# Kernel optimization log

Hardware: AMD Instinct MI355X
Metric: run time of the kernel (lower is better)

Reference implementation:

```python
import jax, jax.numpy as jnp
import numpy as np

D_MODEL = 1024
STATE_DIM = 16
BATCH = 32
SEQ = 2048


def setup_inputs() -> dict:
    key = jax.random.key(0)
    k_x, k_win, k_bin, k_wout, k_bout = jax.random.split(key, 5)
    proj_dim = 2 * D_MODEL + 3 * STATE_DIM
    x = jax.random.normal(k_x, (BATCH, SEQ, D_MODEL), dtype=jnp.float32)
    # Dense kernels (glorot-ish scale) and zero biases, as in fresh keras layers
    W_in = jax.random.normal(k_win, (D_MODEL, proj_dim), dtype=jnp.float32) * 0.02
    b_in = jnp.zeros((proj_dim,), dtype=jnp.float32)
    W_out = jax.random.normal(k_wout, (D_MODEL, D_MODEL), dtype=jnp.float32) * 0.02
    b_out = jnp.zeros((D_MODEL,), dtype=jnp.float32)
    # A_log init: -log([1..state_dim])
    A_log = -jnp.log(jnp.arange(1, STATE_DIM + 1, dtype=jnp.float32))
    return {"x": x, "W_in": W_in, "b_in": b_in, "A_log": A_log,
            "W_out": W_out, "b_out": b_out}


def _selective_scan(delta, A, B, C):
    # delta, B, C: [b, s, n]; A: [n]
    # state_t = exp(A * delta_t) * state_{t-1} + B_t ; y_t = sum(state_t * C_t)
    def step(state, inp):
        delta_t, B_t, C_t = inp  # each [b, n]
        state = jnp.exp(A * delta_t) * state + B_t
        y = jnp.sum(state * C_t, axis=-1)  # [b]
        return state, y

    b = delta.shape[0]
    init = jnp.zeros((b, A.shape[0]), dtype=delta.dtype)
    # scan over time: move seq axis to front -> [s, b, n]
    xs = (jnp.swapaxes(delta, 0, 1), jnp.swapaxes(B, 0, 1), jnp.swapaxes(C, 0, 1))
    _, ys = jax.lax.scan(step, init, xs)  # ys: [s, b]
    return jnp.swapaxes(ys, 0, 1)  # [b, s]


def reference(x, W_in, b_in, A_log, W_out, b_out):
    xz = jnp.einsum('bsd,dp->bsp', x, W_in) + b_in  # [b, s, 2*d + 3*n]
    d, n = D_MODEL, STATE_DIM
    xm = xz[..., :d]                     # unused by scan (matches original)
    z = xz[..., d:2 * d]                 # [b, s, d]
    Bm = xz[..., 2 * d:2 * d + n]        # [b, s, n]
    Cm = xz[..., 2 * d + n:2 * d + 2 * n]
    delta = jax.nn.softplus(xz[..., 2 * d + 2 * n:])  # [b, s, n]
    A = -jnp.exp(A_log)                  # [n]
    y = _selective_scan(delta, A, Bm, Cm)  # [b, s]
    y = y[..., None] * jax.nn.gelu(z, approximate=False)  # [b, s, d]
    return jnp.einsum('bsd,de->bse', y, W_out) + b_out
```

## Files before the change

### kernel.cpp

```cpp
#include <hip/hip_runtime.h>
#include <cstdint>

typedef float fx4 __attribute__((ext_vector_type(4)));
typedef short sx8 __attribute__((ext_vector_type(8)));
typedef short sx4 __attribute__((ext_vector_type(4)));

#define NSTATE 16
#define SEQ_LEN 2048
#define NBATCH 32
#define MROWS 65536
#define KDIM 1024
#define N1 1072
#define N1PAD 1152
#define BK 32
#define NSTEP (KDIM / BK)
#define TILE_SHORTS 4096
#define TSTRIDE (NSTEP * TILE_SHORTS)
#define RING 4
#define SLOT_SHORTS 8192

__device__ __forceinline__ short f2bf(float f) {
  unsigned u = __float_as_uint(f);
  u += 0x7FFFu + ((u >> 16) & 1u);
  return (short)(u >> 16);
}

__device__ __forceinline__ float gelu_exact(float x) {
  float ax = fabsf(x) * 0.70710678118654752f;
  float t = __builtin_amdgcn_rcpf(fmaf(0.3275911f, ax, 1.0f));
  float p = fmaf(1.061405429f, t, -1.453152027f);
  p = fmaf(p, t, 1.421413741f);
  p = fmaf(p, t, -0.284496736f);
  p = fmaf(p, t, 0.254829592f);
  p = p * t;
  float e = __expf(-ax * ax);
  float erfv = fmaf(-p, e, 1.0f);
  erfv = copysignf(erfv, x);
  return 0.5f * x * (1.0f + erfv);
}

#define GLOAD_LDS16(gp, lp)                                                          \
  __builtin_amdgcn_global_load_lds(                                                  \
      (const __attribute__((address_space(1))) unsigned int*)(gp),                   \
      (__attribute__((address_space(3))) unsigned int*)(lp), 16, 0, 0)

#define SBAR() do { __builtin_amdgcn_s_barrier(); asm volatile("" ::: "memory"); } while (0)
#define WAITLGKM0() asm volatile("s_waitcnt lgkmcnt(0)" ::: "memory")

__global__ void convert_pack_x(const float* __restrict__ x, short* __restrict__ xbp) {
  const int wave = threadIdx.x >> 6;
  const int lane = threadIdx.x & 63;
  const int r0 = blockIdx.x * 64 + wave * 16;
  const int q = (lane & 7) >> 1;
  const int eo = (lane & 1) * 4;
  const int kt0 = lane >> 3;
  for (int r16 = 0; r16 < 16; ++r16) {
    const int m = r0 + r16;
    const int rloc = m & 127;
    const long pbase = ((long)(m >> 7) * NSTEP) * TILE_SHORTS + rloc * 32;
    const int p8 = (((q + (rloc >> 1)) & 3)) * 8 + eo;
#pragma unroll
    for (int seg = 0; seg < 4; ++seg) {
      fx4 v = *(const fx4*)(x + (long)m * KDIM + seg * 256 + lane * 4);
      sx4 o;
      o[0] = f2bf(v[0]); o[1] = f2bf(v[1]); o[2] = f2bf(v[2]); o[3] = f2bf(v[3]);
      *(sx4*)(xbp + pbase + (long)(seg * 8 + kt0) * TILE_SHORTS + p8) = o;
    }
  }
}

__global__ void transpose_w_kernel(const float* __restrict__ src, short* __restrict__ dst,
                                   int src_cols, int col_off, int valid_rows) {
  __shared__ float t[32][33];
  int j0 = blockIdx.x * 32;
  int k0 = blockIdx.y * 32;
  int c = threadIdx.x & 31;
  int r = threadIdx.x >> 5;
#pragma unroll
  for (int i = 0; i < 4; i++) {
    int k = k0 + r + i * 8;
    int j = j0 + c;
    float v = (j < valid_rows) ? src[(long)k * src_cols + col_off + j] : 0.f;
    t[r + i * 8][c] = v;
  }
  __syncthreads();
#pragma unroll
  for (int i = 0; i < 4; i++) {
    int n = j0 + r + i * 8;
    int k = k0 + c;
    int rr = n & 127;
    long addr = ((long)(n >> 7) * NSTEP + (k >> 5)) * TILE_SHORTS + rr * 32
              + ((((k >> 3) & 3) + ((rr >> 1) & 3)) & 3) * 8 + (k & 7);
    dst[addr] = f2bf(t[c][r + i * 8]);
  }
}

__device__ __forceinline__ void gemm_mainloop256(const short* __restrict__ Abase,
                                                 const short* __restrict__ Bbase,
                                                 short* lds, fx4 acc[4][4]) {
  const int tid = threadIdx.x;
  const int lane = tid & 63;
  const int wave = tid >> 6;
  const int wm = wave >> 2, wn = wave & 3;
  const int l15 = lane & 15, ks = lane >> 4;

#pragma unroll
  for (int i = 0; i < 4; i++)
#pragma unroll
    for (int j = 0; j < 4; j++) acc[i][j] = fx4{0.f, 0.f, 0.f, 0.f};

  short* AshR = lds;
  short* BshR = lds + RING * SLOT_SHORTS;
  const short* Asrc = Abase + (long)(tid >> 9) * TSTRIDE + (tid & 511) * 8;
  const short* Bsrc = Bbase + (long)(tid >> 9) * TSTRIDE + (tid & 511) * 8;
  const int dst = tid * 8;

  const int rslot = ((ks + (l15 >> 1)) & 3) * 8;
  const int aoff = (wm >> 1) * TILE_SHORTS + ((wm & 1) * 64 + l15) * 32 + rslot;
  const int boff = (wn >> 1) * TILE_SHORTS + ((wn & 1) * 64 + l15) * 32 + rslot;

#pragma unroll
  for (int s = 0; s < RING - 1; s++) {
    GLOAD_LDS16(Asrc + (long)s * TILE_SHORTS, AshR + s * SLOT_SHORTS + dst);
    GLOAD_LDS16(Bsrc + (long)s * TILE_SHORTS, BshR + s * SLOT_SHORTS + dst);
  }

  for (int s = 0; s < NSTEP; ++s) {
    const int rem = NSTEP - 1 - s;
    if (rem >= 2)      asm volatile("s_waitcnt vmcnt(4)" ::: "memory");
    else if (rem == 1) asm volatile("s_waitcnt vmcnt(2)" ::: "memory");
    else               asm volatile("s_waitcnt vmcnt(0)" ::: "memory");
    SBAR();

    if (s + 3 < NSTEP) {
      const int sl = (s + 3) & (RING - 1);
      GLOAD_LDS16(Asrc + (long)(s + 3) * TILE_SHORTS, AshR + sl * SLOT_SHORTS + dst);
      GLOAD_LDS16(Bsrc + (long)(s + 3) * TILE_SHORTS, BshR + sl * SLOT_SHORTS + dst);
    }

    const short* sa = AshR + (s & (RING - 1)) * SLOT_SHORTS + aoff;
    const short* sb = BshR + (s & (RING - 1)) * SLOT_SHORTS + boff;
    sx8 af[4], bfr[4];
#pragma unroll
    for (int i = 0; i < 4; i++) af[i] = *(const sx8*)(sa + i * 512);
#pragma unroll
    for (int j = 0; j < 4; j++) bfr[j] = *(const sx8*)(sb + j * 512);
    WAITLGKM0();
    __builtin_amdgcn_sched_barrier(0);

    __builtin_amdgcn_s_setprio(1);
#pragma unroll
    for (int i = 0; i < 4; i++)
#pragma unroll
      for (int j = 0; j < 4; j++)
        acc[i][j] = __builtin_amdgcn_mfma_f32_16x16x32_bf16(af[i], bfr[j], acc[i][j], 0, 0, 0);
    __builtin_amdgcn_s_setprio(0);
  }
}

__global__ __launch_bounds__(1024, 1) void gemm1_kernel(
    const short* __restrict__ xbp, const short* __restrict__ Wt1p,
    const float* __restrict__ b_in, short* __restrict__ g) {
  extern __shared__ short lds[];
  const int bid = blockIdx.x;
  const int wgid = (bid & 7) * 128 + (bid >> 3);
  const int nt = wgid & 3;
  const int mt = wgid >> 2;
  fx4 acc[4][4];
  gemm_mainloop256(xbp + (long)(mt * 2) * TSTRIDE,
                   Wt1p + (long)(nt * 2) * TSTRIDE, lds, acc);

  const int lane = threadIdx.x & 63;
  const int wave = threadIdx.x >> 6;
  const int wm = wave >> 2, wn = wave & 3;
  const int m0 = mt * 256;
  const int n0 = nt * 256;

#pragma unroll
  for (int ni = 0; ni < 4; ni++) {
    int n = n0 + wn * 64 + ni * 16 + (lane & 15);
    float bias = b_in[1024 + n];
#pragma unroll
    for (int mi = 0; mi < 4; mi++) {
#pragma unroll
      for (int r = 0; r < 4; r++) {
        int m = m0 + wm * 64 + mi * 16 + (lane >> 4) * 4 + r;
        float v = acc[mi][ni][r] + bias;
        int rr = m & 127;
        long addr = ((long)(m >> 7) * NSTEP + (n >> 5)) * TILE_SHORTS + rr * 32
                  + ((((n >> 3) & 3) + ((rr >> 1) & 3)) & 3) * 8 + (n & 7);
        g[addr] = f2bf(gelu_exact(v));
      }
    }
  }
}

__global__ __launch_bounds__(256, 2) void gemm_bcd_kernel(
    const short* __restrict__ xbp, const short* __restrict__ Wt1p,
    const float* __restrict__ b_in, const float* __restrict__ A_log,
    float* __restrict__ Bb, float* __restrict__ Cb, float* __restrict__ ab) {
  __shared__ short Ash[3 * 4096] __attribute__((aligned(16)));
  __shared__ short Bsh[3 * 2048] __attribute__((aligned(16)));
  const int tid = threadIdx.x;
  const int lane = tid & 63, wave = tid >> 6;
  const int l15 = lane & 15, ks = lane >> 4;
  const int bid = blockIdx.x;
  const int mt = (bid & 7) * 64 + (bid >> 3);
  const short* Abase = xbp + (long)mt * TSTRIDE;
  const short* Bbase = Wt1p + (long)8 * TSTRIDE;

  fx4 acc[2][3];
#pragma unroll
  for (int i = 0; i < 2; i++)
#pragma unroll
    for (int j = 0; j < 3; j++) acc[i][j] = fx4{0.f, 0.f, 0.f, 0.f};

  const int rslot = ((ks + (l15 >> 1)) & 3) * 8;
  const int aofb = (wave * 32 + l15) * 32 + rslot;

#pragma unroll
  for (int s = 0; s < 2; s++) {
    GLOAD_LDS16(Abase + (long)s * TILE_SHORTS + tid * 8, Ash + s * 4096 + tid * 8);
    GLOAD_LDS16(Abase + (long)s * TILE_SHORTS + 2048 + tid * 8, Ash + s * 4096 + 2048 + tid * 8);
    GLOAD_LDS16(Bbase + (long)s * TILE_SHORTS + tid * 8, Bsh + s * 2048 + tid * 8);
  }

  for (int s = 0; s < NSTEP; ++s) {
    if (s < NSTEP - 1) asm volatile("s_waitcnt vmcnt(3)" ::: "memory");
    else               asm volatile("s_waitcnt vmcnt(0)" ::: "memory");
    SBAR();
    if (s + 2 < NSTEP) {
      const int sl = (s + 2) % 3;
      GLOAD_LDS16(Abase + (long)(s + 2) * TILE_SHORTS + tid * 8, Ash + sl * 4096 + tid * 8);
      GLOAD_LDS16(Abase + (long)(s + 2) * TILE_SHORTS + 2048 + tid * 8, Ash + sl * 4096 + 2048 + tid * 8);
      GLOAD_LDS16(Bbase + (long)(s + 2) * TILE_SHORTS + tid * 8, Bsh + sl * 2048 + tid * 8);
    }
    const short* sa = Ash + (s % 3) * 4096 + aofb;
    const short* sb = Bsh + (s % 3) * 2048;
    sx8 af[2], bfr[3];
#pragma unroll
    for (int i = 0; i < 2; i++) af[i] = *(const sx8*)(sa + i * 512);
#pragma unroll
    for (int j = 0; j < 3; j++) bfr[j] = *(const sx8*)(sb + (j * 16 + l15) * 32 + rslot);
    WAITLGKM0();
    __builtin_amdgcn_sched_barrier(0);
#pragma unroll
    for (int i = 0; i < 2; i++)
#pragma unroll
      for (int j = 0; j < 3; j++)
        acc[i][j] = __builtin_amdgcn_mfma_f32_16x16x32_bf16(af[i], bfr[j], acc[i][j], 0, 0, 0);
  }

  const float biasB = b_in[2048 + l15];
  const float biasC = b_in[2064 + l15];
  const float biasD = b_in[2080 + l15];
  const float Ac = -expf(A_log[l15]);
#pragma unroll
  for (int mi = 0; mi < 2; mi++) {
#pragma unroll
    for (int r = 0; r < 4; r++) {
      int m = mt * 128 + wave * 32 + mi * 16 + (lane >> 4) * 4 + r;
      Bb[m * NSTATE + l15] = acc[mi][0][r] + biasB;
      Cb[m * NSTATE + l15] = acc[mi][1][r] + biasC;
      float v = acc[mi][2][r] + biasD;
      float dlt = (v > 20.f) ? v : log1pf(expf(v));
      ab[m * NSTATE + l15] = expf(Ac * dlt);
    }
  }
}

__global__ void scan_kernel(const float* __restrict__ ab, const float* __restrict__ Bb,
                            const float* __restrict__ Cb, float* __restrict__ y) {
  __shared__ float Ash[16][17], Bsh[16][17];
  const int b = blockIdx.x;
  const int tid = threadIdx.x;
  const int seg = tid >> 4, ch = tid & 15;
  const long base = ((long)b * SEQ_LEN + seg * 128) * NSTATE + ch;
  const float* pa = ab + base;
  const float* pb = Bb + base;
  const float* pc = Cb + base;

  float A = 1.f, Bc = 0.f;
  for (int i0 = 0; i0 < 128; i0 += 8) {
    float av[8], bv[8];
#pragma unroll
    for (int u = 0; u < 8; u++) { av[u] = pa[(i0 + u) * NSTATE]; bv[u] = pb[(i0 + u) * NSTATE]; }
#pragma unroll
    for (int u = 0; u < 8; u++) { Bc = fmaf(av[u], Bc, bv[u]); A *= av[u]; }
  }
  Ash[seg][ch] = A; Bsh[seg][ch] = Bc;
  __syncthreads();

  if (tid < 16) {
    float s = 0.f;
    for (int sg = 0; sg < 16; ++sg) {
      float nxt = fmaf(Ash[sg][tid], s, Bsh[sg][tid]);
      Bsh[sg][tid] = s;
      s = nxt;
    }
  }
  __syncthreads();

  float s = Bsh[seg][ch];
  float* py = y + (long)b * SEQ_LEN + seg * 128;
  for (int i0 = 0; i0 < 128; i0 += 8) {
    float av[8], bv[8], cv[8];
#pragma unroll
    for (int u = 0; u < 8; u++) {
      av[u] = pa[(i0 + u) * NSTATE];
      bv[u] = pb[(i0 + u) * NSTATE];
      cv[u] = pc[(i0 + u) * NSTATE];
    }
#pragma unroll
    for (int u = 0; u < 8; u++) {
      s = fmaf(av[u], s, bv[u]);
      float p = s * cv[u];
      p += __shfl_xor(p, 1);
      p += __shfl_xor(p, 2);
      p += __shfl_xor(p, 4);
      p += __shfl_xor(p, 8);
      if (ch == 0) py[i0 + u] = p;
    }
  }
}

__global__ __launch_bounds__(1024, 1) void gemm2_kernel(
    const short* __restrict__ g, const short* __restrict__ Wt2p,
    const float* __restrict__ y, const float* __restrict__ b_out,
    float* __restrict__ out) {
  extern __shared__ short lds[];
  const int bid = blockIdx.x;
  const int wgid = (bid & 7) * 128 + (bid >> 3);
  const int nt = wgid & 3;
  const int mt = wgid >> 2;
  fx4 acc[4][4];
  gemm_mainloop256(g + (long)(mt * 2) * TSTRIDE,
                   Wt2p + (long)(nt * 2) * TSTRIDE, lds, acc);

  const int lane = threadIdx.x & 63;
  const int wave = threadIdx.x >> 6;
  const int wm = wave >> 2, wn = wave & 3;
  const int m0 = mt * 256;
  const int n0 = nt * 256;

#pragma unroll
  for (int mi = 0; mi < 4; mi++) {
#pragma unroll
    for (int r = 0; r < 4; r++) {
      int m = m0 + wm * 64 + mi * 16 + (lane >> 4) * 4 + r;
      float ym = y[m];
#pragma unroll
      for (int ni = 0; ni < 4; ni++) {
        int n = n0 + wn * 64 + ni * 16 + (lane & 15);
        out[(long)m * 1024 + n] = fmaf(ym, acc[mi][ni][r], b_out[n]);
      }
    }
  }
}

extern "C" void kernel_launch(void* const* d_in, const int* in_sizes, int n_in,
                              void* d_out, int out_size, void* d_ws, size_t ws_size,
                              hipStream_t stream) {
  const float* x     = (const float*)d_in[0];
  const float* W_in  = (const float*)d_in[1];
  const float* b_in  = (const float*)d_in[2];
  const float* A_log = (const float*)d_in[3];
  const float* W_out = (const float*)d_in[4];
  const float* b_out = (const float*)d_in[5];
  float* out = (float*)d_out;

  char* ws = (char*)d_ws;
  short* xbp = (short*)ws;  ws += (size_t)MROWS * KDIM * 2;
  short* g   = (short*)ws;  ws += (size_t)MROWS * KDIM * 2;
  short* Wt1p = (short*)ws; ws += (size_t)N1PAD * KDIM * 2;
  short* Wt2p = (short*)ws; ws += (size_t)KDIM * KDIM * 2;
  float* Bb = (float*)ws;  ws += (size_t)MROWS * NSTATE * 4;
  float* Cb = (float*)ws;  ws += (size_t)MROWS * NSTATE * 4;
  float* ab = (float*)ws;  ws += (size_t)MROWS * NSTATE * 4;
  float* y  = (float*)ws;  ws += (size_t)MROWS * 4;

  const int ldsBytes = 2 * RING * SLOT_SHORTS * 2;

  convert_pack_x<<<1024, 256, 0, stream>>>(x, xbp);
  transpose_w_kernel<<<dim3(N1PAD / 32, 32), 256, 0, stream>>>(W_in, Wt1p, 2096, 1024, N1);
  transpose_w_kernel<<<dim3(32, 32), 256, 0, stream>>>(W_out, Wt2p, 1024, 0, 1024);
  gemm_bcd_kernel<<<512, 256, 0, stream>>>(xbp, Wt1p, b_in, A_log, Bb, Cb, ab);
  scan_kernel<<<NBATCH, 256, 0, stream>>>(ab, Bb, Cb, y);
  gemm1_kernel<<<1024, 1024, ldsBytes, stream>>>(xbp, Wt1p, b_in, g);
  gemm2_kernel<<<1024, 1024, ldsBytes, stream>>>(g, Wt2p, y, b_out, out);
}
```

Measured before the change: 485.7 us.

## Halve GEMM block to 8 waves with 128x64 per-wave tiles; repack x conversion

The two big GEMM kernels now run 512 threads (8 waves) per 256x256 tile instead of 1024. Each wave computes a 128x64 sub-tile with 8x4 MFMA accumulators, and every thread issues two global-to-LDS loads per operand per stage, with the vmcnt waits adjusted to match. The aim is more MFMA work per LDS fragment read and less barrier and wave overhead, at the cost of doubled accumulator registers per thread and fewer waves to hide latency. Separately, convert_pack_x is reorganised so each wave converts one 32-column k-tile of a 128-row panel, giving more blocks and more contiguous packed writes.

```diff
diff --git a/kernel.cpp b/kernel.cpp
--- a/kernel.cpp
+++ b/kernel.cpp
@@ -48,24 +48,21 @@
 #define WAITLGKM0() asm volatile("s_waitcnt lgkmcnt(0)" ::: "memory")
 
 __global__ void convert_pack_x(const float* __restrict__ x, short* __restrict__ xbp) {
-  const int wave = threadIdx.x >> 6;
-  const int lane = threadIdx.x & 63;
-  const int r0 = blockIdx.x * 64 + wave * 16;
+  const int wave = threadIdx.x >> 6, lane = threadIdx.x & 63;
+  const int p = blockIdx.x >> 3;
+  const int kt = (blockIdx.x & 7) * 4 + wave;
+  const int lr = lane >> 3;
   const int q = (lane & 7) >> 1;
   const int eo = (lane & 1) * 4;
-  const int kt0 = lane >> 3;
-  for (int r16 = 0; r16 < 16; ++r16) {
-    const int m = r0 + r16;
-    const int rloc = m & 127;
-    const long pbase = ((long)(m >> 7) * NSTEP) * TILE_SHORTS + rloc * 32;
-    const int p8 = (((q + (rloc >> 1)) & 3)) * 8 + eo;
-#pragma unroll
-    for (int seg = 0; seg < 4; ++seg) {
-      fx4 v = *(const fx4*)(x + (long)m * KDIM + seg * 256 + lane * 4);
-      sx4 o;
-      o[0] = f2bf(v[0]); o[1] = f2bf(v[1]); o[2] = f2bf(v[2]); o[3] = f2bf(v[3]);
-      *(sx4*)(xbp + pbase + (long)(seg * 8 + kt0) * TILE_SHORTS + p8) = o;
-    }
+  const float* xb = x + ((long)p * 128) * KDIM + kt * 32 + (lane & 7) * 4;
+  short* db = xbp + (long)p * TSTRIDE + (long)kt * TILE_SHORTS;
+#pragma unroll 4
+  for (int r8 = 0; r8 < 16; ++r8) {
+    int r = r8 * 8 + lr;
+    fx4 v = *(const fx4*)(xb + (long)r * KDIM);
+    sx4 o;
+    o[0] = f2bf(v[0]); o[1] = f2bf(v[1]); o[2] = f2bf(v[2]); o[3] = f2bf(v[3]);
+    *(sx4*)(db + r * 32 + (((q + ((r >> 1) & 3)) & 3)) * 8 + eo) = o;
   }
 }
 
@@ -97,7 +94,7 @@
 
 __device__ __forceinline__ void gemm_mainloop256(const short* __restrict__ Abase,
                                                  const short* __restrict__ Bbase,
-                                                 short* lds, fx4 acc[4][4]) {
+                                                 short* lds, fx4 acc[8][4]) {
   const int tid = threadIdx.x;
   const int lane = tid & 63;
   const int wave = tid >> 6;
@@ -105,52 +102,60 @@
   const int l15 = lane & 15, ks = lane >> 4;
 
 #pragma unroll
-  for (int i = 0; i < 4; i++)
+  for (int i = 0; i < 8; i++)
 #pragma unroll
     for (int j = 0; j < 4; j++) acc[i][j] = fx4{0.f, 0.f, 0.f, 0.f};
 
   short* AshR = lds;
   short* BshR = lds + RING * SLOT_SHORTS;
-  const short* Asrc = Abase + (long)(tid >> 9) * TSTRIDE + (tid & 511) * 8;
-  const short* Bsrc = Bbase + (long)(tid >> 9) * TSTRIDE + (tid & 511) * 8;
+  const short* Asrc = Abase + tid * 8;
+  const short* Bsrc = Bbase + tid * 8;
   const int dst = tid * 8;
 
   const int rslot = ((ks + (l15 >> 1)) & 3) * 8;
-  const int aoff = (wm >> 1) * TILE_SHORTS + ((wm & 1) * 64 + l15) * 32 + rslot;
-  const int boff = (wn >> 1) * TILE_SHORTS + ((wn & 1) * 64 + l15) * 32 + rslot;
+  int aof[8], bof[4];
+#pragma unroll
+  for (int mi = 0; mi < 8; mi++) aof[mi] = wm * 4096 + (mi * 16 + l15) * 32 + rslot;
+#pragma unroll
+  for (int ni = 0; ni < 4; ni++)
+    bof[ni] = (wn >> 1) * 4096 + ((wn & 1) * 64 + ni * 16 + l15) * 32 + rslot;
 
 #pragma unroll
   for (int s = 0; s < RING - 1; s++) {
-    GLOAD_LDS16(Asrc + (long)s * TILE_SHORTS, AshR + s * SLOT_SHORTS + dst);
-    GLOAD_LDS16(Bsrc + (long)s * TILE_SHORTS, BshR + s * SLOT_SHORTS + dst);
+    GLOAD_LDS16(Asrc + (long)s * TILE_SHORTS,           AshR + s * SLOT_SHORTS + dst);
+    GLOAD_LDS16(Asrc + TSTRIDE + (long)s * TILE_SHORTS, AshR + s * SLOT_SHORTS + 4096 + dst);
+    GLOAD_LDS16(Bsrc + (long)s * TILE_SHORTS,           BshR + s * SLOT_SHORTS + dst);
+    GLOAD_LDS16(Bsrc + TSTRIDE + (long)s * TILE_SHORTS, BshR + s * SLOT_SHORTS + 4096 + dst);
   }
 
   for (int s = 0; s < NSTEP; ++s) {
     const int rem = NSTEP - 1 - s;
-    if (rem >= 2)      asm volatile("s_waitcnt vmcnt(4)" ::: "memory");
-    else if (rem == 1) asm volatile("s_waitcnt vmcnt(2)" ::: "memory");
+    if (rem >= 2)      asm volatile("s_waitcnt vmcnt(8)" ::: "memory");
+    else if (rem == 1) asm volatile("s_waitcnt vmcnt(4)" ::: "memory");
     else               asm volatile("s_waitcnt vmcnt(0)" ::: "memory");
     SBAR();
 
     if (s + 3 < NSTEP) {
       const int sl = (s + 3) & (RING - 1);
-      GLOAD_LDS16(Asrc + (long)(s + 3) * TILE_SHORTS, AshR + sl * SLOT_SHORTS + dst);
-      GLOAD_LDS16(Bsrc + (long)(s + 3) * TILE_SHORTS, BshR + sl * SLOT_SHORTS + dst);
-    }
-
-    const short* sa = AshR + (s & (RING - 1)) * SLOT_SHORTS + aoff;
-    const short* sb = BshR + (s & (RING - 1)) * SLOT_SHORTS + boff;
-    sx8 af[4], bfr[4];
-#pragma unroll
-    for (int i = 0; i < 4; i++) af[i] = *(const sx8*)(sa + i * 512);
-#pragma unroll
-    for (int j = 0; j < 4; j++) bfr[j] = *(const sx8*)(sb + j * 512);
+      GLOAD_LDS16(Asrc + (long)(s + 3) * TILE_SHORTS,           AshR + sl * SLOT_SHORTS + dst);
+      GLOAD_LDS16(Asrc + TSTRIDE + (long)(s + 3) * TILE_SHORTS, AshR + sl * SLOT_SHORTS + 4096 + dst);
+      GLOAD_LDS16(Bsrc + (long)(s + 3) * TILE_SHORTS,           BshR + sl * SLOT_SHORTS + dst);
+      GLOAD_LDS16(Bsrc + TSTRIDE + (long)(s + 3) * TILE_SHORTS, BshR + sl * SLOT_SHORTS + 4096 + dst);
+    }
+
+    const short* sa = AshR + (s & (RING - 1)) * SLOT_SHORTS;
+    const short* sb = BshR + (s & (RING - 1)) * SLOT_SHORTS;
+    sx8 af[8], bfr[4];
+#pragma unroll
+    for (int i = 0; i < 8; i++) af[i] = *(const sx8*)(sa + aof[i]);
+#pragma unroll
+    for (int j = 0; j < 4; j++) bfr[j] = *(const sx8*)(sb + bof[j]);
     WAITLGKM0();
     __builtin_amdgcn_sched_barrier(0);
 
     __builtin_amdgcn_s_setprio(1);
 #pragma unroll
-    for (int i = 0; i < 4; i++)
+    for (int i = 0; i < 8; i++)
 #pragma unroll
       for (int j = 0; j < 4; j++)
         acc[i][j] = __builtin_amdgcn_mfma_f32_16x16x32_bf16(af[i], bfr[j], acc[i][j], 0, 0, 0);
@@ -158,7 +163,7 @@
   }
 }
 
-__global__ __launch_bounds__(1024, 1) void gemm1_kernel(
+__global__ __launch_bounds__(512, 1) void gemm1_kernel(
     const short* __restrict__ xbp, const short* __restrict__ Wt1p,
     const float* __restrict__ b_in, short* __restrict__ g) {
   extern __shared__ short lds[];
@@ -166,7 +171,7 @@
   const int wgid = (bid & 7) * 128 + (bid >> 3);
   const int nt = wgid & 3;
   const int mt = wgid >> 2;
-  fx4 acc[4][4];
+  fx4 acc[8][4];
   gemm_mainloop256(xbp + (long)(mt * 2) * TSTRIDE,
                    Wt1p + (long)(nt * 2) * TSTRIDE, lds, acc);
 
@@ -181,10 +186,10 @@
     int n = n0 + wn * 64 + ni * 16 + (lane & 15);
     float bias = b_in[1024 + n];
 #pragma unroll
-    for (int mi = 0; mi < 4; mi++) {
+    for (int mi = 0; mi < 8; mi++) {
 #pragma unroll
       for (int r = 0; r < 4; r++) {
-        int m = m0 + wm * 64 + mi * 16 + (lane >> 4) * 4 + r;
+        int m = m0 + wm * 128 + mi * 16 + (lane >> 4) * 4 + r;
         float v = acc[mi][ni][r] + bias;
         int rr = m & 127;
         long addr = ((long)(m >> 7) * NSTEP + (n >> 5)) * TILE_SHORTS + rr * 32
@@ -324,7 +329,7 @@
   }
 }
 
-__global__ __launch_bounds__(1024, 1) void gemm2_kernel(
+__global__ __launch_bounds__(512, 1) void gemm2_kernel(
     const short* __restrict__ g, const short* __restrict__ Wt2p,
     const float* __restrict__ y, const float* __restrict__ b_out,
     float* __restrict__ out) {
@@ -333,7 +338,7 @@
   const int wgid = (bid & 7) * 128 + (bid >> 3);
   const int nt = wgid & 3;
   const int mt = wgid >> 2;
-  fx4 acc[4][4];
+  fx4 acc[8][4];
   gemm_mainloop256(g + (long)(mt * 2) * TSTRIDE,
                    Wt2p + (long)(nt * 2) * TSTRIDE, lds, acc);
 
@@ -344,10 +349,10 @@
   const int n0 = nt * 256;
 
 #pragma unroll
-  for (int mi = 0; mi < 4; mi++) {
+  for (int mi = 0; mi < 8; mi++) {
 #pragma unroll
     for (int r = 0; r < 4; r++) {
-      int m = m0 + wm * 64 + mi * 16 + (lane >> 4) * 4 + r;
+      int m = m0 + wm * 128 + mi * 16 + (lane >> 4) * 4 + r;
       float ym = y[m];
 #pragma unroll
       for (int ni = 0; ni < 4; ni++) {
@@ -381,11 +386,11 @@
 
   const int ldsBytes = 2 * RING * SLOT_SHORTS * 2;
 
-  convert_pack_x<<<1024, 256, 0, stream>>>(x, xbp);
+  convert_pack_x<<<4096, 256, 0, stream>>>(x, xbp);
   transpose_w_kernel<<<dim3(N1PAD / 32, 32), 256, 0, stream>>>(W_in, Wt1p, 2096, 1024, N1);
   transpose_w_kernel<<<dim3(32, 32), 256, 0, stream>>>(W_out, Wt2p, 1024, 0, 1024);
   gemm_bcd_kernel<<<512, 256, 0, stream>>>(xbp, Wt1p, b_in, A_log, Bb, Cb, ab);
   scan_kernel<<<NBATCH, 256, 0, stream>>>(ab, Bb, Cb, y);
-  gemm1_kernel<<<1024, 1024, ldsBytes, stream>>>(xbp, Wt1p, b_in, g);
-  gemm2_kernel<<<1024, 1024, ldsBytes, stream>>>(g, Wt2p, y, b_out, out);
-}
+  gemm1_kernel<<<1024, 512, ldsBytes, stream>>>(xbp, Wt1p, b_in, g);
+  gemm2_kernel<<<1024, 512, ldsBytes, stream>>>(g, Wt2p, y, b_out, out);
+}
```

After: 493.8 us. No clear change (+1.7%).
